# Optimization experiments

Hardware: AMD Instinct MI355X
Metric: run time of the kernel (lower is better)

Reference implementation:

```python
import jax, jax.numpy as jnp
import numpy as np

K = 3
STRIDE = 1
PAD = 1


def conv2d(x, w, b):
    # standard NCHW conv, stride 1, pad 1
    out = jax.lax.conv_general_dilated(
        x, w, (STRIDE, STRIDE), [(PAD, PAD), (PAD, PAD)],
        dimension_numbers=("NCHW", "OIHW", "NCHW"))
    return out + b[None, :, None, None]


def deform_conv2d(x, offset, mask, weight):
    # torchvision.ops.deform_conv2d semantics (offset_groups=1):
    # offset: [B, 2*K*K, Ho, Wo] laid out as (k, (y, x)) per kernel tap k (row-major)
    # mask:   [B, K*K, Ho, Wo]
    B, C, H, W = x.shape
    KK = K * K
    Ho, Wo = offset.shape[2:]
    off = offset.reshape(B, KK, 2, Ho, Wo)

    # base sampling positions: p = out*stride - pad + kernel_tap + offset
    tap_y = jnp.repeat(jnp.arange(K, dtype=x.dtype), K)  # [KK]
    tap_x = jnp.tile(jnp.arange(K, dtype=x.dtype), K)    # [KK]
    grid_y = jnp.arange(Ho, dtype=x.dtype) * STRIDE - PAD
    grid_x = jnp.arange(Wo, dtype=x.dtype) * STRIDE - PAD
    py = grid_y[None, None, :, None] + tap_y[None, :, None, None] + off[:, :, 0]  # [B,KK,Ho,Wo]
    px = grid_x[None, None, None, :] + tap_x[None, :, None, None] + off[:, :, 1]

    y0 = jnp.floor(py)
    x0 = jnp.floor(px)
    wy1 = py - y0  # fractional parts
    wx1 = px - x0

    xf = x.reshape(B, C, H * W)

    def gather(yi, xi):
        # zero-padding semantics: out-of-bounds corners contribute 0
        valid = (yi >= 0) & (yi <= H - 1) & (xi >= 0) & (xi <= W - 1)
        idx = (jnp.clip(yi, 0, H - 1) * W + jnp.clip(xi, 0, W - 1)).astype(jnp.int32)
        v = jnp.take_along_axis(xf, idx.reshape(B, 1, KK * Ho * Wo), axis=2)
        v = v.reshape(B, C, KK, Ho, Wo)
        return v * valid[:, None].astype(x.dtype)

    e = lambda a: a[:, None]  # [B,KK,Ho,Wo] -> [B,1,KK,Ho,Wo]
    sampled = (gather(y0, x0) * e((1 - wy1) * (1 - wx1))
               + gather(y0, x0 + 1) * e((1 - wy1) * wx1)
               + gather(y0 + 1, x0) * e(wy1 * (1 - wx1))
               + gather(y0 + 1, x0 + 1) * e(wy1 * wx1))
    sampled = sampled * mask[:, None]  # modulated, [B,C,KK,Ho,Wo]

    Cout = weight.shape[0]
    out = jnp.einsum("bckhw,ock->bohw", sampled, weight.reshape(Cout, C, KK))
    return out


def setup_inputs() -> dict:
    key = jax.random.key(0)
    ks = jax.random.split(key, 5)
    B, Cin, Cout, H, W = 4, 128, 256, 64, 64
    x = jax.random.normal(ks[0], (B, Cin, H, W), jnp.float32)
    # offset/modulator convs are zero-init in the module; use small random weights
    # so the deformable sampling path is actually exercised
    offset_w = jax.random.normal(ks[1], (2 * K * K, Cin, K, K), jnp.float32) * 0.02
    offset_b = jax.random.normal(ks[2], (2 * K * K,), jnp.float32) * 0.1
    mod_w = jax.random.normal(ks[3], (K * K, Cin, K, K), jnp.float32) * 0.02
    mod_b = jnp.zeros((K * K,), jnp.float32)
    weight = jax.random.normal(ks[4], (Cout, Cin, K, K), jnp.float32) * (1.0 / np.sqrt(Cin * K * K))
    return {"x": x, "offset_w": offset_w, "offset_b": offset_b,
            "mod_w": mod_w, "mod_b": mod_b, "weight": weight}


def reference(x, offset_w, offset_b, mod_w, mod_b, weight):
    H, W = x.shape[2], x.shape[3]
    max_offset = max(H, W) / 4.0
    offset = jnp.clip(conv2d(x, offset_w, offset_b), -max_offset, max_offset)
    mask = 2.0 * jax.nn.sigmoid(conv2d(x, mod_w, mod_b))
    return deform_conv2d(x, offset, mask, weight)
```

## Files before the change

### kernel.cpp

```cpp
#include <hip/hip_runtime.h>
#include <math.h>

#define CIN   128
#define COUT  256
#define HH    64
#define WW    64
#define BB    4
#define KK    9
#define CK    (CIN*KK)

typedef unsigned short u16;
typedef unsigned int   u32;
using f32x4  = __attribute__((ext_vector_type(4))) float;
using s16x8  = __attribute__((ext_vector_type(8))) short;

__device__ __forceinline__ u16 f2bf(float f) {
    union { float f; u32 u; } v; v.f = f;
    u32 u = v.u;
    u += 0x7FFFu + ((u >> 16) & 1u);
    return (u16)(u >> 16);
}
__device__ __forceinline__ float bfel(s16x8 v, int j) {
    union { u32 u; float f; } c; c.u = ((u32)(u16)v[j]) << 16; return c.f;
}
__device__ __forceinline__ u32 asu(float f) {
    union { float f; u32 u; } v; v.f = f; return v.u;
}

__global__ __launch_bounds__(256)
void prep_all(const float* __restrict__ x, const float* __restrict__ w,
              const float* __restrict__ ow, const float* __restrict__ mw,
              u16* __restrict__ xt, u16* __restrict__ wfrag,
              u16* __restrict__ wofsf) {
    __shared__ u16 T[64][130];
    int blk = blockIdx.x;
    int tid = threadIdx.x;

    if (blk < 256) {
        int b = blk >> 6, y = blk & 63;
        int lane = tid & 63, cw = tid >> 6;
        for (int c = cw; c < 128; c += 4)
            T[lane][c] = f2bf(x[((b * 128 + c) * 64 + y) * 64 + lane]);
        __syncthreads();
        int c = tid & 127;
        for (int p = tid >> 7; p < 64; p += 2)
            xt[((b * 64 + y) * 64 + p) * 128 + c] = T[p][c];
    } else if (blk < 256 + 1152) {
        int i = (blk - 256) * 256 + tid;
        int j    = i & 7;
        int lane = (i >> 3) & 63;
        int ks4  = (i >> 9) & 3;
        int t    = (i >> 11) & 1;
        int wv   = (i >> 12) & 7;
        int tap  = i >> 15;
        int co = (wv * 2 + t) * 16 + (lane & 15);
        int k  = tap * 128 + ks4 * 32 + (lane >> 4) * 8 + j;
        int c  = k & 127;
        wfrag[i] = f2bf(w[co * CK + c * 9 + tap]);
    } else {
        int i = (blk - 1408) * 256 + tid;
        if (i < 9 * 4096) {
            int j    = i & 7;
            int lane = (i >> 3) & 63;
            int ks4  = (i >> 9) & 3;
            int t    = (i >> 11) & 1;
            int tap  = i >> 12;
            int co = t * 16 + (lane & 15);
            int k  = tap * 128 + ks4 * 32 + (lane >> 4) * 8 + j;
            int c  = k & 127;
            float v = 0.f;
            if (co < 18)      v = ow[co * CK + c * 9 + tap];
            else if (co < 27) v = mw[(co - 18) * CK + c * 9 + tap];
            wofsf[i] = f2bf(v);
        }
    }
}

__global__ __launch_bounds__(512, 2)
void dcn_fused(const u16* __restrict__ xt, const u16* __restrict__ wofsf,
               const float* __restrict__ ob, const float* __restrict__ mb,
               const u16* __restrict__ wfrag, float* __restrict__ out) {
    int blkid = blockIdx.x;
    int xcd = blkid & 7, idx = blkid >> 3;
    int b   = xcd >> 1;
    int ho  = ((xcd & 1) << 5) + idx;
    int tid = threadIdx.x;

    __shared__ __align__(16) u16 Sm[2][64][136];
    __shared__ float s_om[27][64];
    __shared__ int   s_idx[64][KK][4];
    __shared__ float s_wgt[64][KK][4];

    int wv   = tid >> 6, lane = tid & 63;
    int quad = lane >> 4, l16 = lane & 15;
    int p2   = (wv * 4 + quad) * 2;

    const u16* xtb = xt + (size_t)b * 4096 * 128;
    const s16x8 vzero = {0,0,0,0,0,0,0,0};

    {
        int t  = wv & 1;
        int ph = wv >> 1;
        f32x4 aco = (f32x4)(0.f);
        int col0 = ph * 16 + l16 - 1;
#pragma unroll
        for (int tap = 0; tap < KK; ++tap) {
            int y   = ho - 1 + tap / 3;
            int col = col0 + tap % 3;
            bool ok = ((unsigned)y < HH) && ((unsigned)col < WW);
            int yc = ((unsigned)y < HH) ? y : 0;
            int cc = ((unsigned)col < WW) ? col : 0;
            const u16* src = xtb + (size_t)(yc * 64 + cc) * 128 + quad * 8;
            const u16* wc  = wofsf + tap * 4096 + t * 2048 + lane * 8;
#pragma unroll
            for (int ks4 = 0; ks4 < 4; ++ks4) {
                s16x8 bf = *(const s16x8*)(src + ks4 * 32);
                bf = ok ? bf : vzero;
                s16x8 af = *(const s16x8*)(wc + ks4 * 512);
                aco = __builtin_amdgcn_mfma_f32_16x16x32_bf16(af, bf, aco, 0, 0, 0);
            }
        }
#pragma unroll
        for (int r = 0; r < 4; ++r) {
            int co = t * 16 + quad * 4 + r;
            if (co < 27) {
                float v = aco[r];
                if (co < 18) {
                    v += ob[co];
                    v = fminf(fmaxf(v, -16.f), 16.f);
                } else {
                    v += mb[co - 18];
                    v = 2.f / (1.f + expf(-v));
                }
                s_om[co][ph * 16 + l16] = v;
            }
        }
    }
    __syncthreads();

    for (int i = tid; i < 64 * KK; i += 512) {
        int p = i / KK, k = i - (i / KK) * KK;
        int wo = p;
        float offy = s_om[2 * k][p];
        float offx = s_om[2 * k + 1][p];
        float mval = s_om[18 + k][p];

        float py = (float)(ho - 1 + k / 3) + offy;
        float px = (float)(wo - 1 + k % 3) + offx;
        float y0f = floorf(py), x0f = floorf(px);
        float wy1 = py - y0f,  wx1 = px - x0f;
        float wy0 = 1.f - wy1, wx0 = 1.f - wx1;
        int iy0 = (int)y0f, ix0 = (int)x0f;
        int iy1 = iy0 + 1,  ix1 = ix0 + 1;
        bool vy0 = (iy0 >= 0) && (iy0 < HH);
        bool vy1 = (iy1 >= 0) && (iy1 < HH);
        bool vx0 = (ix0 >= 0) && (ix0 < WW);
        bool vx1 = (ix1 >= 0) && (ix1 < WW);
        int cy0 = min(max(iy0, 0), HH - 1), cy1 = min(max(iy1, 0), HH - 1);
        int cx0 = min(max(ix0, 0), WW - 1), cx1 = min(max(ix1, 0), WW - 1);
        s_idx[p][k][0] = (cy0 * WW + cx0) * 128;
        s_idx[p][k][1] = (cy0 * WW + cx1) * 128;
        s_idx[p][k][2] = (cy1 * WW + cx0) * 128;
        s_idx[p][k][3] = (cy1 * WW + cx1) * 128;
        s_wgt[p][k][0] = (vy0 && vx0) ? mval * wy0 * wx0 : 0.f;
        s_wgt[p][k][1] = (vy0 && vx1) ? mval * wy0 * wx1 : 0.f;
        s_wgt[p][k][2] = (vy1 && vx0) ? mval * wy1 * wx0 : 0.f;
        s_wgt[p][k][3] = (vy1 && vx1) ? mval * wy1 * wx1 : 0.f;
    }
    __syncthreads();

    f32x4 acc[2][4];
#pragma unroll
    for (int t = 0; t < 2; ++t)
#pragma unroll
        for (int ph = 0; ph < 4; ++ph) acc[t][ph] = (f32x4)(0.f);

    s16x8 crs[2][2][4];
    float gs[2][2][4];
    s16x8 afp[8];

    auto gatherB = [&](int tap, int sp) {
#pragma unroll
        for (int e = 0; e < 2; ++e) {
            int p = p2 + e;
            int i0 = s_idx[p][tap][0], i1 = s_idx[p][tap][1];
            int i2 = s_idx[p][tap][2], i3 = s_idx[p][tap][3];
            gs[sp][e][0] = s_wgt[p][tap][0]; gs[sp][e][1] = s_wgt[p][tap][1];
            gs[sp][e][2] = s_wgt[p][tap][2]; gs[sp][e][3] = s_wgt[p][tap][3];
            int co8 = l16 * 8;
            crs[sp][e][0] = *(const s16x8*)(xtb + i0 + co8);
            crs[sp][e][1] = *(const s16x8*)(xtb + i1 + co8);
            crs[sp][e][2] = *(const s16x8*)(xtb + i2 + co8);
            crs[sp][e][3] = *(const s16x8*)(xtb + i3 + co8);
        }
    };

    auto blend_store = [&](int sp) {
#pragma unroll
        for (int e = 0; e < 2; ++e) {
            float g0 = gs[sp][e][0], g1 = gs[sp][e][1];
            float g2 = gs[sp][e][2], g3 = gs[sp][e][3];
            float o[8];
#pragma unroll
            for (int j = 0; j < 8; ++j)
                o[j] = g0 * bfel(crs[sp][e][0], j) + g1 * bfel(crs[sp][e][1], j)
                     + g2 * bfel(crs[sp][e][2], j) + g3 * bfel(crs[sp][e][3], j);
            uint4 pkv;
            pkv.x = (asu(o[1]) & 0xFFFF0000u) | (asu(o[0]) >> 16);
            pkv.y = (asu(o[3]) & 0xFFFF0000u) | (asu(o[2]) >> 16);
            pkv.z = (asu(o[5]) & 0xFFFF0000u) | (asu(o[4]) >> 16);
            pkv.w = (asu(o[7]) & 0xFFFF0000u) | (asu(o[6]) >> 16);
            *(uint4*)(&Sm[sp][p2 + e][l16 * 8]) = pkv;
        }
    };

    auto af_prefetch = [&](int tap) {
        const u16* wc = wfrag + (tap * 8 + wv) * 4096 + lane * 8;
#pragma unroll
        for (int t = 0; t < 2; ++t)
#pragma unroll
            for (int ks4 = 0; ks4 < 4; ++ks4)
                afp[t * 4 + ks4] = *(const s16x8*)(wc + (t * 4 + ks4) * 512);
    };

    auto pb_mfma_tap = [&](int sp) {
#pragma unroll
        for (int ks4 = 0; ks4 < 4; ++ks4) {
            s16x8 bf[4];
#pragma unroll
            for (int ph = 0; ph < 4; ++ph)
                bf[ph] = *(const s16x8*)(&Sm[sp][ph * 16 + l16][ks4 * 32 + quad * 8]);
#pragma unroll
            for (int t = 0; t < 2; ++t)
#pragma unroll
                for (int ph = 0; ph < 4; ++ph)
                    acc[t][ph] = __builtin_amdgcn_mfma_f32_16x16x32_bf16(afp[t * 4 + ks4], bf[ph], acc[t][ph], 0, 0, 0);
        }
    };

    gatherB(0, 0);
#pragma unroll
    for (int tap = 0; tap < KK; ++tap) {
        int sp = tap & 1;
        blend_store(sp);
        af_prefetch(tap);
        __syncthreads();
        if (tap < KK - 1) gatherB(tap + 1, sp ^ 1);
        pb_mfma_tap(sp);
    }

#pragma unroll
    for (int t = 0; t < 2; ++t) {
        int cobase = (wv * 2 + t) * 16 + quad * 4;
#pragma unroll
        for (int ph = 0; ph < 4; ++ph) {
#pragma unroll
            for (int r = 0; r < 4; ++r) {
                int co = cobase + r;
                out[((b * COUT + co) * HH + ho) * WW + ph * 16 + l16] = acc[t][ph][r];
            }
        }
    }
}

extern "C" void kernel_launch(void* const* d_in, const int* in_sizes, int n_in,
                              void* d_out, int out_size, void* d_ws, size_t ws_size,
                              hipStream_t stream) {
    const float* x  = (const float*)d_in[0];
    const float* ow = (const float*)d_in[1];
    const float* ob = (const float*)d_in[2];
    const float* mw = (const float*)d_in[3];
    const float* mb = (const float*)d_in[4];
    const float* wt = (const float*)d_in[5];

    char* ws = (char*)d_ws;
    u16* wfrag = (u16*)ws;  ws += (size_t)COUT * CK * 2;
    u16* wofsf = (u16*)ws;  ws += (size_t)32 * CK * 2;
    u16* xt    = (u16*)ws;
    float* out = (float*)d_out;

    prep_all<<<1552, 256, 0, stream>>>(x, wt, ow, mw, xt, wfrag, wofsf);

    dcn_fused<<<BB * HH, 512, 0, stream>>>(xt, wofsf, ob, mb, wfrag, out);
}
```

Baseline: 101.8 us.

## Fuse prep and DCN kernels into one cooperative launch with grid sync

Merges the bf16 conversion and transpose of x, weight fragment packing, and the main deformable conv into a single cooperative kernel. Each of the 256 blocks converts its own input row and a strided share of the weights, then a grid-wide barrier separates prep from compute. This removes one kernel launch and the gap between launches. In exchange it adds a grid sync, a larger shared-memory footprint (extra transpose buffer) that may hurt occupancy, and a requirement that all blocks are co-resident.

```diff
diff --git a/kernel.cpp b/kernel.cpp
--- a/kernel.cpp
+++ b/kernel.cpp
@@ -1,4 +1,5 @@
 #include <hip/hip_runtime.h>
+#include <hip/hip_cooperative_groups.h>
 #include <math.h>
 
 #define CIN   128
@@ -27,69 +28,63 @@
     union { float f; u32 u; } v; v.f = f; return v.u;
 }
 
-__global__ __launch_bounds__(256)
-void prep_all(const float* __restrict__ x, const float* __restrict__ w,
-              const float* __restrict__ ow, const float* __restrict__ mw,
-              u16* __restrict__ xt, u16* __restrict__ wfrag,
-              u16* __restrict__ wofsf) {
-    __shared__ u16 T[64][130];
-    int blk = blockIdx.x;
-    int tid = threadIdx.x;
-
-    if (blk < 256) {
-        int b = blk >> 6, y = blk & 63;
-        int lane = tid & 63, cw = tid >> 6;
-        for (int c = cw; c < 128; c += 4)
-            T[lane][c] = f2bf(x[((b * 128 + c) * 64 + y) * 64 + lane]);
-        __syncthreads();
-        int c = tid & 127;
-        for (int p = tid >> 7; p < 64; p += 2)
-            xt[((b * 64 + y) * 64 + p) * 128 + c] = T[p][c];
-    } else if (blk < 256 + 1152) {
-        int i = (blk - 256) * 256 + tid;
-        int j    = i & 7;
-        int lane = (i >> 3) & 63;
-        int ks4  = (i >> 9) & 3;
-        int t    = (i >> 11) & 1;
-        int wv   = (i >> 12) & 7;
-        int tap  = i >> 15;
-        int co = (wv * 2 + t) * 16 + (lane & 15);
-        int k  = tap * 128 + ks4 * 32 + (lane >> 4) * 8 + j;
-        int c  = k & 127;
-        wfrag[i] = f2bf(w[co * CK + c * 9 + tap]);
-    } else {
-        int i = (blk - 1408) * 256 + tid;
-        if (i < 9 * 4096) {
-            int j    = i & 7;
-            int lane = (i >> 3) & 63;
-            int ks4  = (i >> 9) & 3;
-            int t    = (i >> 11) & 1;
-            int tap  = i >> 12;
-            int co = t * 16 + (lane & 15);
-            int k  = tap * 128 + ks4 * 32 + (lane >> 4) * 8 + j;
-            int c  = k & 127;
-            float v = 0.f;
-            if (co < 18)      v = ow[co * CK + c * 9 + tap];
-            else if (co < 27) v = mw[(co - 18) * CK + c * 9 + tap];
-            wofsf[i] = f2bf(v);
-        }
-    }
-}
-
 __global__ __launch_bounds__(512, 2)
-void dcn_fused(const u16* __restrict__ xt, const u16* __restrict__ wofsf,
-               const float* __restrict__ ob, const float* __restrict__ mb,
-               const u16* __restrict__ wfrag, float* __restrict__ out) {
+void dcn_all(const float* __restrict__ x, const float* __restrict__ ow,
+             const float* __restrict__ ob, const float* __restrict__ mw,
+             const float* __restrict__ mb, const float* __restrict__ wt,
+             u16* __restrict__ xt, u16* __restrict__ wofsf,
+             u16* __restrict__ wfrag, float* __restrict__ out) {
     int blkid = blockIdx.x;
     int xcd = blkid & 7, idx = blkid >> 3;
     int b   = xcd >> 1;
     int ho  = ((xcd & 1) << 5) + idx;
     int tid = threadIdx.x;
 
+    __shared__ u16 T[64][130];
     __shared__ __align__(16) u16 Sm[2][64][136];
     __shared__ float s_om[27][64];
     __shared__ int   s_idx[64][KK][4];
     __shared__ float s_wgt[64][KK][4];
+
+    {
+        int lane = tid & 63, cw = tid >> 6;
+        for (int c = cw; c < 128; c += 8)
+            T[lane][c] = f2bf(x[((b * 128 + c) * 64 + ho) * 64 + lane]);
+        __syncthreads();
+        int c = tid & 127;
+        for (int p = tid >> 7; p < 64; p += 4)
+            xt[((b * 64 + ho) * 64 + p) * 128 + c] = T[p][c];
+
+        int g = blkid * 512 + tid;
+        for (int i = g; i < COUT * CK; i += 256 * 512) {
+            int j    = i & 7;
+            int ln   = (i >> 3) & 63;
+            int ks4  = (i >> 9) & 3;
+            int t    = (i >> 11) & 1;
+            int wv2  = (i >> 12) & 7;
+            int tap  = i >> 15;
+            int co = (wv2 * 2 + t) * 16 + (ln & 15);
+            int k  = tap * 128 + ks4 * 32 + (ln >> 4) * 8 + j;
+            int cc = k & 127;
+            wfrag[i] = f2bf(wt[co * CK + cc * 9 + tap]);
+        }
+        if (g < 9 * 4096) {
+            int i = g;
+            int j    = i & 7;
+            int ln   = (i >> 3) & 63;
+            int ks4  = (i >> 9) & 3;
+            int t    = (i >> 11) & 1;
+            int tap  = i >> 12;
+            int co = t * 16 + (ln & 15);
+            int k  = tap * 128 + ks4 * 32 + (ln >> 4) * 8 + j;
+            int cc = k & 127;
+            float v = 0.f;
+            if (co < 18)      v = ow[co * CK + cc * 9 + tap];
+            else if (co < 27) v = mw[(co - 18) * CK + cc * 9 + tap];
+            wofsf[i] = f2bf(v);
+        }
+    }
+    cooperative_groups::this_grid().sync();
 
     int wv   = tid >> 6, lane = tid & 63;
     int quad = lane >> 4, l16 = lane & 15;
@@ -140,13 +135,12 @@
 
     for (int i = tid; i < 64 * KK; i += 512) {
         int p = i / KK, k = i - (i / KK) * KK;
-        int wo = p;
         float offy = s_om[2 * k][p];
         float offx = s_om[2 * k + 1][p];
         float mval = s_om[18 + k][p];
 
         float py = (float)(ho - 1 + k / 3) + offy;
-        float px = (float)(wo - 1 + k % 3) + offx;
+        float px = (float)(p - 1 + k % 3) + offx;
         float y0f = floorf(py), x0f = floorf(px);
         float wy1 = py - y0f,  wx1 = px - x0f;
         float wy0 = 1.f - wy1, wx0 = 1.f - wx1;
@@ -279,7 +273,8 @@
     u16* xt    = (u16*)ws;
     float* out = (float*)d_out;
 
-    prep_all<<<1552, 256, 0, stream>>>(x, wt, ow, mw, xt, wfrag, wofsf);
-
-    dcn_fused<<<BB * HH, 512, 0, stream>>>(xt, wofsf, ob, mb, wfrag, out);
-}
+    void* args[] = {(void*)&x, (void*)&ow, (void*)&ob, (void*)&mw, (void*)&mb,
+                    (void*)&wt, (void*)&xt, (void*)&wofsf, (void*)&wfrag, (void*)&out};
+    hipLaunchCooperativeKernel((const void*)dcn_all, dim3(BB * HH), dim3(512),
+                               args, 0, stream);
+}
```

Result: slower. 151.2 us (+48.5%).
